# Optimization experiments

Measured on AMD Instinct MI355X. Metric: run time of the kernel, lower is better.

Reference implementation:

```python
import jax, jax.numpy as jnp
import numpy as np

IN_FEATURES = 8192
OUT_FEATURES = 8192
POOL_K = 16
SCALE = 2.0


def setup_inputs() -> dict:
    key = jax.random.key(0)
    k1, k2, k3 = jax.random.split(key, 3)
    B = 4096
    x = jax.random.normal(k1, (B, IN_FEATURES), dtype=jnp.float32)
    # nn.Linear default init: U(-1/sqrt(fan_in), 1/sqrt(fan_in))
    bound = 1.0 / np.sqrt(IN_FEATURES)
    W = jax.random.uniform(k2, (OUT_FEATURES, IN_FEATURES), dtype=jnp.float32, minval=-bound, maxval=bound)
    b = jax.random.uniform(k3, (OUT_FEATURES,), dtype=jnp.float32, minval=-bound, maxval=bound)
    return {"x": x, "W": W, "b": b}


def reference(x, W, b):
    # GEMM: [B, C_out]
    y = jnp.dot(x, W.T) + b
    B, C = y.shape
    # AvgPool1d over feature dim, kernel=stride=POOL_K -> [B, C/POOL_K]
    pooled = y.reshape(B, C // POOL_K, POOL_K).mean(axis=-1)
    # GELU (tanh approximation) + scale, then row-wise max -> [B]
    v = jax.nn.gelu(pooled, approximate=True) * SCALE
    return jnp.max(v, axis=-1)
```

## Files before the change

kernel.cpp:

```cpp
#include <hip/hip_runtime.h>
#include <hip/hip_bf16.h>
#include <cmath>

#define M_DIM 4096
#define N_POOL 512
#define K_DIM 8192
#define KSPLIT 8
#define K_PER (K_DIM / KSPLIT)

typedef __bf16 bf16x8 __attribute__((ext_vector_type(8)));
typedef float floatx4 __attribute__((ext_vector_type(4)));
typedef unsigned short ushort8v __attribute__((ext_vector_type(8)));

__device__ __forceinline__ unsigned short f2bf(float f) {
  unsigned int u = __float_as_uint(f);
  return (unsigned short)((u + 0x7fffu + ((u >> 16) & 1u)) >> 16);
}

#define WPOOL_BLOCKS 512
#define CONV_BLOCKS 2048

__global__ __launch_bounds__(256) void prep_kernel(
    const float* __restrict__ W, unsigned short* __restrict__ Wp,
    const float4* __restrict__ src, ushort8v* __restrict__ dst, int n8,
    const float* __restrict__ b, float* __restrict__ bpool) {
  int bid = blockIdx.x;
  if (bid < WPOOL_BLOCKS) {
    int g = bid;
    const float* base = W + (size_t)g * 16 * K_DIM;
    ushort4* out = (ushort4*)(Wp + (size_t)g * K_DIM);
    for (int c4 = threadIdx.x; c4 < K_DIM / 4; c4 += blockDim.x) {
      float4 s = {0.f, 0.f, 0.f, 0.f};
#pragma unroll
      for (int j = 0; j < 16; ++j) {
        float4 v = ((const float4*)(base + (size_t)j * K_DIM))[c4];
        s.x += v.x; s.y += v.y; s.z += v.z; s.w += v.w;
      }
      ushort4 o;
      o.x = f2bf(s.x); o.y = f2bf(s.y); o.z = f2bf(s.z); o.w = f2bf(s.w);
      out[c4] = o;
    }
  } else if (bid < WPOOL_BLOCKS + CONV_BLOCKS) {
    int i = (bid - WPOOL_BLOCKS) * blockDim.x + threadIdx.x;
    int stride = CONV_BLOCKS * blockDim.x;
    for (; i < n8; i += stride) {
      float4 a = src[2 * i], c = src[2 * i + 1];
      ushort8v o;
      o[0] = f2bf(a.x); o[1] = f2bf(a.y); o[2] = f2bf(a.z); o[3] = f2bf(a.w);
      o[4] = f2bf(c.x); o[5] = f2bf(c.y); o[6] = f2bf(c.z); o[7] = f2bf(c.w);
      dst[i] = o;
    }
  } else {
    for (int g = threadIdx.x; g < N_POOL; g += blockDim.x) {
      float s = 0.f;
#pragma unroll
      for (int i = 0; i < 16; ++i) s += b[g * 16 + i];
      bpool[g] = s;
    }
  }
}

__global__ __launch_bounds__(256) void gemm_splitk(
    const unsigned short* __restrict__ xb,
    const unsigned short* __restrict__ wp,
    float* __restrict__ part)
{
  __shared__ __align__(16) unsigned short As[128 * 64];
  __shared__ __align__(16) unsigned short Bs[128 * 64];

  const int tid = threadIdx.x;
  const int L = tid & 63;
  const int w = tid >> 6;
  const int wm = w & 1, wn = w >> 1;
  const int lane15 = L & 15, quad = L >> 4;

  const int id = blockIdx.x;
  const int kz = id & 7;
  const int c = id >> 3;
  const int bn = c & 3, bm = c >> 2;

  const int srow = w * 32 + (L >> 3);
  const int schunk = ((L & 7) ^ ((L >> 3) & 7)) * 8;
  const unsigned short* ga = xb + (size_t)(bm * 128 + srow) * K_DIM + kz * K_PER + schunk;
  const unsigned short* gb = wp + (size_t)(bn * 128 + srow) * K_DIM + kz * K_PER + schunk;
  unsigned short* lA = As + (w * 32) * 64;
  unsigned short* lB = Bs + (w * 32) * 64;

  floatx4 acc[4][4];
#pragma unroll
  for (int t = 0; t < 4; ++t)
#pragma unroll
    for (int u = 0; u < 4; ++u) acc[t][u] = (floatx4)0.f;

  const bf16x8* Av = (const bf16x8*)As;
  const bf16x8* Bv = (const bf16x8*)Bs;

  for (int kk = 0; kk < K_PER / 64; ++kk) {
#pragma unroll
    for (int i = 0; i < 4; ++i) {
      __builtin_amdgcn_global_load_lds(
          (const __attribute__((address_space(1))) void*)(ga + (size_t)(i * 8) * K_DIM),
          (__attribute__((address_space(3))) void*)(lA + i * 8 * 64), 16, 0, 0);
    }
#pragma unroll
    for (int i = 0; i < 4; ++i) {
      __builtin_amdgcn_global_load_lds(
          (const __attribute__((address_space(1))) void*)(gb + (size_t)(i * 8) * K_DIM),
          (__attribute__((address_space(3))) void*)(lB + i * 8 * 64), 16, 0, 0);
    }
    ga += 64; gb += 64;
    __syncthreads();

#pragma unroll
    for (int ks = 0; ks < 2; ++ks) {
      bf16x8 af[4], bfr[4];
#pragma unroll
      for (int t = 0; t < 4; ++t) {
        int r = wm * 64 + t * 16 + lane15;
        af[t] = Av[r * 8 + ((ks * 4 + quad) ^ (lane15 & 7))];
      }
#pragma unroll
      for (int u = 0; u < 4; ++u) {
        int r = wn * 64 + u * 16 + lane15;
        bfr[u] = Bv[r * 8 + ((ks * 4 + quad) ^ (lane15 & 7))];
      }
#pragma unroll
      for (int t = 0; t < 4; ++t)
#pragma unroll
        for (int u = 0; u < 4; ++u)
          acc[t][u] = __builtin_amdgcn_mfma_f32_16x16x32_bf16(af[t], bfr[u],
                                                              acc[t][u], 0, 0, 0);
    }
    __syncthreads();
  }

  float* cp = part + (size_t)kz * M_DIM * N_POOL;
  const int row_base = bm * 128 + wm * 64;
  const int col_base = bn * 128 + wn * 64;
#pragma unroll
  for (int t = 0; t < 4; ++t)
#pragma unroll
    for (int u = 0; u < 4; ++u) {
      int col = col_base + u * 16 + lane15;
#pragma unroll
      for (int r = 0; r < 4; ++r) {
        int row = row_base + t * 16 + quad * 4 + r;
        cp[(size_t)row * N_POOL + col] = acc[t][u][r];
      }
    }
}

__device__ __forceinline__ float gelu2(float s) {
  float p = s * 0.0625f;
  float t = tanhf(0.7978845608028654f * (p + 0.044715f * p * p * p));
  return p * (1.0f + t);
}

__global__ void finalize(const float* __restrict__ part,
                         const float* __restrict__ bpool,
                         float* __restrict__ out) {
  const int w = threadIdx.x >> 6, lane = threadIdx.x & 63;
  const int row = blockIdx.x * 4 + w;
  const float4* bp4 = (const float4*)bpool;
  float mx = -INFINITY;
#pragma unroll
  for (int j = 0; j < 2; ++j) {
    int g4 = lane + j * 64;
    float4 s = bp4[g4];
#pragma unroll
    for (int kz = 0; kz < KSPLIT; ++kz) {
      float4 v = ((const float4*)(part + (size_t)kz * M_DIM * N_POOL +
                                  (size_t)row * N_POOL))[g4];
      s.x += v.x; s.y += v.y; s.z += v.z; s.w += v.w;
    }
    mx = fmaxf(mx, fmaxf(fmaxf(gelu2(s.x), gelu2(s.y)),
                         fmaxf(gelu2(s.z), gelu2(s.w))));
  }
#pragma unroll
  for (int sh = 32; sh >= 1; sh >>= 1) mx = fmaxf(mx, __shfl_xor(mx, sh));
  if (lane == 0) out[row] = mx;
}

extern "C" void kernel_launch(void* const* d_in, const int* in_sizes, int n_in,
                              void* d_out, int out_size, void* d_ws, size_t ws_size,
                              hipStream_t stream) {
  const float* x = (const float*)d_in[0];
  const float* W = (const float*)d_in[1];
  const float* b = (const float*)d_in[2];
  float* out = (float*)d_out;

  char* ws = (char*)d_ws;
  unsigned short* xb = (unsigned short*)ws;
  unsigned short* Wp = (unsigned short*)(ws + (size_t)67108864);
  float* part = (float*)(ws + (size_t)75497472);
  float* bpool = (float*)(ws + (size_t)142606336);

  prep_kernel<<<WPOOL_BLOCKS + CONV_BLOCKS + 1, 256, 0, stream>>>(
      W, Wp, (const float4*)x, (ushort8v*)xb, (M_DIM * K_DIM) / 8, b, bpool);

  gemm_splitk<<<1024, 256, 0, stream>>>(xb, Wp, part);

  finalize<<<M_DIM / 4, 256, 0, stream>>>(part, bpool, out);
}
```

Before: 502.6 us.

## Fuse x fp32-to-bf16 conversion into GEMM tile loads and halve split-K

Drops the separate pass that converted x to bf16 in the workspace. The GEMM now loads fp32 x tiles into registers, packs them to bf16 with v_cvt_pk_bf16_f32, and stores them into LDS, while W still goes through direct global-to-LDS loads. Split-K is reduced from 8 to 4 and block indices are remapped so that tiles sharing data land on the same XCD, which shrinks the partial-sum buffer. The aim is to remove the extra read and write of x. The cost is twice the global bytes per x tile, register-staged loads that are no longer asynchronous, and only 512 blocks in the grid.

```diff
diff --git a/kernel.cpp b/kernel.cpp
--- a/kernel.cpp
+++ b/kernel.cpp
@@ -5,27 +5,22 @@
 #define M_DIM 4096
 #define N_POOL 512
 #define K_DIM 8192
-#define KSPLIT 8
+#define KSPLIT 4
 #define K_PER (K_DIM / KSPLIT)
 
 typedef __bf16 bf16x8 __attribute__((ext_vector_type(8)));
 typedef float floatx4 __attribute__((ext_vector_type(4)));
-typedef unsigned short ushort8v __attribute__((ext_vector_type(8)));
 
 __device__ __forceinline__ unsigned short f2bf(float f) {
   unsigned int u = __float_as_uint(f);
   return (unsigned short)((u + 0x7fffu + ((u >> 16) & 1u)) >> 16);
 }
 
-#define WPOOL_BLOCKS 512
-#define CONV_BLOCKS 2048
-
 __global__ __launch_bounds__(256) void prep_kernel(
     const float* __restrict__ W, unsigned short* __restrict__ Wp,
-    const float4* __restrict__ src, ushort8v* __restrict__ dst, int n8,
     const float* __restrict__ b, float* __restrict__ bpool) {
   int bid = blockIdx.x;
-  if (bid < WPOOL_BLOCKS) {
+  if (bid < N_POOL) {
     int g = bid;
     const float* base = W + (size_t)g * 16 * K_DIM;
     ushort4* out = (ushort4*)(Wp + (size_t)g * K_DIM);
@@ -40,16 +35,6 @@
       o.x = f2bf(s.x); o.y = f2bf(s.y); o.z = f2bf(s.z); o.w = f2bf(s.w);
       out[c4] = o;
     }
-  } else if (bid < WPOOL_BLOCKS + CONV_BLOCKS) {
-    int i = (bid - WPOOL_BLOCKS) * blockDim.x + threadIdx.x;
-    int stride = CONV_BLOCKS * blockDim.x;
-    for (; i < n8; i += stride) {
-      float4 a = src[2 * i], c = src[2 * i + 1];
-      ushort8v o;
-      o[0] = f2bf(a.x); o[1] = f2bf(a.y); o[2] = f2bf(a.z); o[3] = f2bf(a.w);
-      o[4] = f2bf(c.x); o[5] = f2bf(c.y); o[6] = f2bf(c.z); o[7] = f2bf(c.w);
-      dst[i] = o;
-    }
   } else {
     for (int g = threadIdx.x; g < N_POOL; g += blockDim.x) {
       float s = 0.f;
@@ -61,7 +46,7 @@
 }
 
 __global__ __launch_bounds__(256) void gemm_splitk(
-    const unsigned short* __restrict__ xb,
+    const float* __restrict__ x,
     const unsigned short* __restrict__ wp,
     float* __restrict__ part)
 {
@@ -75,15 +60,17 @@
   const int lane15 = L & 15, quad = L >> 4;
 
   const int id = blockIdx.x;
-  const int kz = id & 7;
+  const int xcd = id & 7;
   const int c = id >> 3;
-  const int bn = c & 3, bm = c >> 2;
+  const int kz = xcd >> 1;
+  const int j = (c << 1) | (xcd & 1);
+  const int bn = j & 3, bm = j >> 2;
 
   const int srow = w * 32 + (L >> 3);
-  const int schunk = ((L & 7) ^ ((L >> 3) & 7)) * 8;
-  const unsigned short* ga = xb + (size_t)(bm * 128 + srow) * K_DIM + kz * K_PER + schunk;
-  const unsigned short* gb = wp + (size_t)(bn * 128 + srow) * K_DIM + kz * K_PER + schunk;
-  unsigned short* lA = As + (w * 32) * 64;
+  const int gcol8 = (L & 7) ^ ((L >> 3) & 7);
+  const float* gx = x + (size_t)(bm * 128 + srow) * K_DIM + kz * K_PER + gcol8 * 8;
+  const unsigned short* gb = wp + (size_t)(bn * 128 + srow) * K_DIM + kz * K_PER + gcol8 * 8;
+  unsigned short* wA = As + srow * 64 + (L & 7) * 8;
   unsigned short* lB = Bs + (w * 32) * 64;
 
   floatx4 acc[4][4];
@@ -96,11 +83,12 @@
   const bf16x8* Bv = (const bf16x8*)Bs;
 
   for (int kk = 0; kk < K_PER / 64; ++kk) {
+    float4 fa[4], fb4[4];
 #pragma unroll
     for (int i = 0; i < 4; ++i) {
-      __builtin_amdgcn_global_load_lds(
-          (const __attribute__((address_space(1))) void*)(ga + (size_t)(i * 8) * K_DIM),
-          (__attribute__((address_space(3))) void*)(lA + i * 8 * 64), 16, 0, 0);
+      const float4* p = (const float4*)(gx + (size_t)(i * 8) * K_DIM);
+      fa[i] = p[0];
+      fb4[i] = p[1];
     }
 #pragma unroll
     for (int i = 0; i < 4; ++i) {
@@ -108,7 +96,16 @@
           (const __attribute__((address_space(1))) void*)(gb + (size_t)(i * 8) * K_DIM),
           (__attribute__((address_space(3))) void*)(lB + i * 8 * 64), 16, 0, 0);
     }
-    ga += 64; gb += 64;
+    gx += 64; gb += 64;
+#pragma unroll
+    for (int i = 0; i < 4; ++i) {
+      uint4 o;
+      asm("v_cvt_pk_bf16_f32 %0, %1, %2" : "=v"(o.x) : "v"(fa[i].x), "v"(fa[i].y));
+      asm("v_cvt_pk_bf16_f32 %0, %1, %2" : "=v"(o.y) : "v"(fa[i].z), "v"(fa[i].w));
+      asm("v_cvt_pk_bf16_f32 %0, %1, %2" : "=v"(o.z) : "v"(fb4[i].x), "v"(fb4[i].y));
+      asm("v_cvt_pk_bf16_f32 %0, %1, %2" : "=v"(o.w) : "v"(fb4[i].z), "v"(fb4[i].w));
+      *(uint4*)(wA + (size_t)(i * 8) * 64) = o;
+    }
     __syncthreads();
 
 #pragma unroll
@@ -190,15 +187,13 @@
   float* out = (float*)d_out;
 
   char* ws = (char*)d_ws;
-  unsigned short* xb = (unsigned short*)ws;
-  unsigned short* Wp = (unsigned short*)(ws + (size_t)67108864);
-  float* part = (float*)(ws + (size_t)75497472);
-  float* bpool = (float*)(ws + (size_t)142606336);
+  unsigned short* Wp = (unsigned short*)ws;
+  float* part = (float*)(ws + (size_t)8388608);
+  float* bpool = (float*)(ws + (size_t)41943040);
 
-  prep_kernel<<<WPOOL_BLOCKS + CONV_BLOCKS + 1, 256, 0, stream>>>(
-      W, Wp, (const float4*)x, (ushort8v*)xb, (M_DIM * K_DIM) / 8, b, bpool);
+  prep_kernel<<<N_POOL + 1, 256, 0, stream>>>(W, Wp, b, bpool);
 
-  gemm_splitk<<<1024, 256, 0, stream>>>(xb, Wp, part);
+  gemm_splitk<<<512, 256, 0, stream>>>(x, Wp, part);
 
   finalize<<<M_DIM / 4, 256, 0, stream>>>(part, bpool, out);
 }
```

New measurement: 475.3 us. -5.4%, faster.
